# Performance work log

Hardware: AMD Instinct MI355X
Metric: run time of the kernel (lower is better)

The kernel has to match this reference:

```python
import jax, jax.numpy as jnp
import numpy as np

DIM = 1024
HEADS = 16


def setup_inputs() -> dict:
    key = jax.random.key(0)
    ks = jax.random.split(key, 5)
    x = jax.random.normal(ks[0], (2, 2048, DIM), dtype=jnp.float32)
    # nn.Linear init-like scaling
    qkv_w = jax.random.normal(ks[1], (3 * DIM, DIM), dtype=jnp.float32) * (1.0 / np.sqrt(DIM))
    qkv_b = jax.random.normal(ks[2], (3 * DIM,), dtype=jnp.float32) * 0.02
    proj_w = jax.random.normal(ks[3], (DIM, DIM), dtype=jnp.float32) * (1.0 / np.sqrt(DIM))
    proj_b = jax.random.normal(ks[4], (DIM,), dtype=jnp.float32) * 0.02
    return {"x": x, "qkv_w": qkv_w, "qkv_b": qkv_b, "proj_w": proj_w, "proj_b": proj_b}


def reference(x, qkv_w, qkv_b, proj_w, proj_b):
    B, N, C = x.shape
    H = HEADS
    Dh = C // H
    scale = Dh ** -0.5
    # qkv: [B, N, 3C] -> [3, B, H, N, Dh]
    qkv = (x @ qkv_w.T + qkv_b).reshape(B, N, 3, H, Dh).transpose(2, 0, 3, 1, 4)
    q, k, v = qkv[0], qkv[1], qkv[2]
    attn = jnp.einsum('bhnd,bhmd->bhnm', q, k) * scale
    attn = jax.nn.softmax(attn, axis=-1)
    out = jnp.einsum('bhnm,bhmd->bhnd', attn, v)  # [B, H, N, Dh]
    out = out.transpose(0, 2, 1, 3).reshape(B, N, C)
    return out @ proj_w.T + proj_b
```

## Files before the change

### kernel.cpp

```cpp
#include <hip/hip_runtime.h>
#include <stdint.h>

#define DIM    1024
#define NHEADS 16
#define DH     64
#define SEQ    2048
#define BATCH  2
#define BHEADS (BATCH * NHEADS)
#define MROWS  (BATCH * SEQ)
#define SL2E   0.18033688011112042f

typedef __attribute__((ext_vector_type(8))) short bf16x8;
typedef __attribute__((ext_vector_type(4))) float f32x4;
typedef unsigned short ushort_t;

#define GLDS(gp, lp) __builtin_amdgcn_global_load_lds( \
    (__attribute__((address_space(1))) void*)(gp), \
    (__attribute__((address_space(3))) void*)(lp), 16, 0, 0)

__device__ inline ushort_t f2bf(float f) {
    unsigned u = __builtin_bit_cast(unsigned, f);
    u += 0x7FFFu + ((u >> 16) & 1u);
    return (ushort_t)(u >> 16);
}

__global__ __launch_bounds__(256) void cvt_kernel(
    const float* __restrict__ s0, const float* __restrict__ s1, const float* __restrict__ s2,
    ushort_t* __restrict__ d0, ushort_t* __restrict__ d1, ushort_t* __restrict__ d2)
{
    const int N0 = MROWS * DIM;
    const int N1 = 3 * DIM * DIM;
    const int N2 = DIM * DIM;
    int e = (blockIdx.x * 256 + threadIdx.x) << 2;
    const float* src; ushort_t* dst;
    if (e < N0)                { src = s0 + e;             dst = d0 + e; }
    else if (e < N0 + N1)      { src = s1 + (e - N0);      dst = d1 + (e - N0); }
    else if (e < N0 + N1 + N2) { src = s2 + (e - N0 - N1); dst = d2 + (e - N0 - N1); }
    else return;
    float4 f = *(const float4*)src;
    ushort4 o;
    o.x = f2bf(f.x); o.y = f2bf(f.y); o.z = f2bf(f.z); o.w = f2bf(f.w);
    *(ushort4*)dst = o;
}

__global__ __launch_bounds__(256) void qkv_gemm(
    const ushort_t* __restrict__ A, const ushort_t* __restrict__ W,
    const float* __restrict__ bias,
    ushort_t* __restrict__ Qw, ushort_t* __restrict__ Kw, ushort_t* __restrict__ Vt)
{
    __shared__ ushort_t smem[128 * 136];
    ushort_t* As = smem;
    ushort_t* Bs = smem + 128 * 64;

    const int tid  = threadIdx.x;
    const int lane = tid & 63;
    const int wave = tid >> 6;
    const int quad = lane >> 4;
    const int l16  = lane & 15;
    const int wm   = (wave >> 1) * 64;
    const int wn   = (wave & 1) * 64;
    const int bm   = blockIdx.x * 128;
    const int bn   = blockIdx.y * 128;
    const int Rl   = lane >> 3;
    const int pp   = lane & 7;

    f32x4 acc[4][4];
    for (int i = 0; i < 4; i++)
        for (int j = 0; j < 4; j++)
            for (int r = 0; r < 4; r++) acc[i][j][r] = 0.f;

    for (int kk = 0; kk < DIM; kk += 64) {
        __syncthreads();
        for (int j = 0; j < 4; j++) {
            int Rb = j * 32 + wave * 8;
            int R  = Rb + Rl;
            int c  = pp ^ (R & 7);
            GLDS(A + (size_t)(bm + R) * DIM + kk + c * 8, As + Rb * 64 + lane * 8);
            GLDS(W + (size_t)(bn + R) * DIM + kk + c * 8, Bs + Rb * 64 + lane * 8);
        }
        __syncthreads();

        for (int kh = 0; kh < 2; kh++) {
            bf16x8 a[4], b[4];
            for (int mi = 0; mi < 4; mi++) {
                int r = wm + mi * 16 + l16;
                a[mi] = *(const bf16x8*)(As + r * 64 + (((kh * 4 + quad) ^ (r & 7)) << 3));
            }
            for (int ni = 0; ni < 4; ni++) {
                int r = wn + ni * 16 + l16;
                b[ni] = *(const bf16x8*)(Bs + r * 64 + (((kh * 4 + quad) ^ (r & 7)) << 3));
            }
            for (int mi = 0; mi < 4; mi++)
                for (int ni = 0; ni < 4; ni++)
                    acc[mi][ni] = __builtin_amdgcn_mfma_f32_16x16x32_bf16(a[mi], b[ni], acc[mi][ni], 0, 0, 0);
        }
    }

    __syncthreads();
    const int three = bn >> 10;
    const float scale = (three == 0) ? SL2E : 1.0f;
    for (int ni = 0; ni < 4; ni++) {
        int cl   = wn + ni * 16 + l16;
        float bv = bias[bn + cl];
        for (int mi = 0; mi < 4; mi++)
            for (int reg = 0; reg < 4; reg++) {
                int r = wm + mi * 16 + quad * 4 + reg;
                smem[r * 136 + cl] = f2bf((acc[mi][ni][reg] + bv) * scale);
            }
    }
    __syncthreads();

    const int b = bm >> 11, npos0 = bm & 2047;
    if (three < 2) {
        int r = tid >> 1, hh = tid & 1;
        int hc = (bn + hh * 64) & 1023;
        int h  = hc >> 6;
        ushort_t* dst = (three == 0 ? Qw : Kw) + ((size_t)(b * NHEADS + h) * SEQ + npos0 + r) * DH;
        const ushort_t* srcp = smem + r * 136 + hh * 64;
        for (int s = 0; s < 8; s++)
            *(uint4*)(dst + s * 8) = *(const uint4*)(srcp + s * 8);
    } else {
        int c = tid & 127, hh = tid >> 7;
        int hc = (bn + c) & 1023;
        int h  = hc >> 6, d = hc & 63;
        ushort_t* dst = Vt + ((size_t)(b * NHEADS + h) * DH + d) * SEQ + npos0 + hh * 64;
        for (int s = 0; s < 8; s++) {
            union { ushort_t u[8]; uint4 v; } tmp;
            for (int k2 = 0; k2 < 8; k2++)
                tmp.u[k2] = smem[(hh * 64 + s * 8 + k2) * 136 + c];
            *(uint4*)(dst + s * 8) = tmp.v;
        }
    }
}

__global__ __launch_bounds__(512, 4) void attn_kernel(
    const ushort_t* __restrict__ Qw, const ushort_t* __restrict__ Kw,
    const ushort_t* __restrict__ Vt, ushort_t* __restrict__ Ao)
{
    __shared__ ushort_t KV[3][2][64 * 64];
    __shared__ ushort_t QP[8 * 32 * 64];

    const int tid  = threadIdx.x;
    const int lane = tid & 63;
    const int wave = tid >> 6;
    const int quad = lane >> 4;
    const int l16  = lane & 15;
    const int bh   = blockIdx.y;
    const int q0   = blockIdx.x * 256;
    const int Rl   = lane >> 3;
    const int pp   = lane & 7;

    const ushort_t* Qh = Qw + (size_t)bh * SEQ * DH;
    const ushort_t* Kh = Kw + (size_t)bh * SEQ * DH;
    const ushort_t* Vh = Vt + (size_t)bh * DH * SEQ;

    for (int j = 0; j < 4; j++) {
        int Rb = j * 64 + wave * 8;
        int R  = Rb + Rl;
        int c  = pp ^ (R & 7);
        GLDS(Qh + (size_t)(q0 + R) * DH + c * 8, QP + Rb * 64 + lane * 8);
    }
    for (int t = 0; t < 2; t++) {
        int Rb = wave * 8;
        int R  = Rb + Rl;
        int c  = pp ^ (R & 7);
        GLDS(Kh + (size_t)(t * 64 + R) * DH + c * 8,  KV[t][0] + Rb * 64 + lane * 8);
        GLDS(Vh + (size_t)R * SEQ + t * 64 + c * 8,   KV[t][1] + Rb * 64 + lane * 8);
    }
    __syncthreads();

    bf16x8 qf[2][2];
    for (int mi = 0; mi < 2; mi++)
        for (int kh = 0; kh < 2; kh++) {
            int r = wave * 32 + mi * 16 + l16;
            qf[mi][kh] = *(const bf16x8*)(QP + r * 64 + (((kh * 4 + quad) ^ (r & 7)) << 3));
        }
    __syncthreads();

    bf16x8 vones;
    for (int i = 0; i < 8; i++) vones[i] = (short)0x3F80;

    f32x4 oacc[2][4], liacc[2];
    for (int mi = 0; mi < 2; mi++) {
        for (int r = 0; r < 4; r++) liacc[mi][r] = 0.f;
        for (int d = 0; d < 4; d++)
            for (int r = 0; r < 4; r++) oacc[mi][d][r] = 0.f;
    }

    ushort_t* Pw = QP + wave * 32 * 64;

    const int NT = SEQ / 64;
    int cur = 0;
    for (int jt = 0; jt < NT; jt++) {
        if (jt < NT - 2) {
            int pidx = cur + 2; if (pidx >= 3) pidx -= 3;
            int nj0  = (jt + 2) * 64;
            int Rb = wave * 8;
            int R  = Rb + Rl;
            int c  = pp ^ (R & 7);
            GLDS(Kh + (size_t)(nj0 + R) * DH + c * 8,  KV[pidx][0] + Rb * 64 + lane * 8);
            GLDS(Vh + (size_t)R * SEQ + nj0 + c * 8,   KV[pidx][1] + Rb * 64 + lane * 8);
        }
        const ushort_t* Ksb = KV[cur][0];
        const ushort_t* Vsb = KV[cur][1];

        f32x4 s[2][4];
        for (int mi = 0; mi < 2; mi++)
            for (int nf = 0; nf < 4; nf++)
                for (int r = 0; r < 4; r++) s[mi][nf][r] = 0.f;
        for (int kh = 0; kh < 2; kh++)
            for (int nf = 0; nf < 4; nf++) {
                int r = nf * 16 + l16;
                bf16x8 kf = *(const bf16x8*)(Ksb + r * 64 + (((kh * 4 + quad) ^ (r & 7)) << 3));
                s[0][nf] = __builtin_amdgcn_mfma_f32_16x16x32_bf16(kf, qf[0][kh], s[0][nf], 0, 0, 0);
                s[1][nf] = __builtin_amdgcn_mfma_f32_16x16x32_bf16(kf, qf[1][kh], s[1][nf], 0, 0, 0);
            }

        for (int mi = 0; mi < 2; mi++) {
            int row = mi * 16 + l16;
            for (int nf = 0; nf < 4; nf++) {
                unsigned u0 = __builtin_bit_cast(unsigned, __builtin_amdgcn_exp2f(s[mi][nf][0])) + 0x8000u;
                unsigned u1 = __builtin_bit_cast(unsigned, __builtin_amdgcn_exp2f(s[mi][nf][1])) + 0x8000u;
                unsigned u2 = __builtin_bit_cast(unsigned, __builtin_amdgcn_exp2f(s[mi][nf][2])) + 0x8000u;
                unsigned u3 = __builtin_bit_cast(unsigned, __builtin_amdgcn_exp2f(s[mi][nf][3])) + 0x8000u;
                uint2 pk;
                pk.x = __builtin_amdgcn_perm(u1, u0, 0x07060302u);
                pk.y = __builtin_amdgcn_perm(u3, u2, 0x07060302u);
                int j0 = 2 * nf + (quad >> 1);
                int jp = j0 ^ (row & 7);
                *(uint2*)(Pw + row * 64 + jp * 8 + (quad & 1) * 4) = pk;
            }
        }

        bf16x8 pf[2][2];
        for (int mi = 0; mi < 2; mi++) {
            int row = mi * 16 + l16;
            for (int kh = 0; kh < 2; kh++) {
                int jp = (kh * 4 + quad) ^ (row & 7);
                pf[mi][kh] = *(const bf16x8*)(Pw + row * 64 + jp * 8);
            }
        }

        for (int mi = 0; mi < 2; mi++) {
            liacc[mi] = __builtin_amdgcn_mfma_f32_16x16x32_bf16(pf[mi][0], vones, liacc[mi], 0, 0, 0);
            liacc[mi] = __builtin_amdgcn_mfma_f32_16x16x32_bf16(pf[mi][1], vones, liacc[mi], 0, 0, 0);
        }
        for (int kh = 0; kh < 2; kh++)
            for (int df = 0; df < 4; df++) {
                int r = df * 16 + l16;
                bf16x8 vf = *(const bf16x8*)(Vsb + r * 64 + (((kh * 4 + quad) ^ (r & 7)) << 3));
                oacc[0][df] = __builtin_amdgcn_mfma_f32_16x16x32_bf16(pf[0][kh], vf, oacc[0][df], 0, 0, 0);
                oacc[1][df] = __builtin_amdgcn_mfma_f32_16x16x32_bf16(pf[1][kh], vf, oacc[1][df], 0, 0, 0);
            }

        if (jt < NT - 2) {
            __asm volatile("s_waitcnt vmcnt(2)" ::: "memory");
        } else {
            __asm volatile("s_waitcnt vmcnt(0)" ::: "memory");
        }
        __asm volatile("s_barrier" ::: "memory");

        cur++; if (cur == 3) cur = 0;
    }

    const int b = bh >> 4, h = bh & 15;
    for (int mi = 0; mi < 2; mi++)
        for (int r = 0; r < 4; r++) {
            float inv = 1.0f / liacc[mi][r];
            int row = q0 + wave * 32 + mi * 16 + quad * 4 + r;
            for (int df = 0; df < 4; df++) {
                int col = h * 64 + df * 16 + l16;
                Ao[((size_t)b * SEQ + row) * DIM + col] = f2bf(oacc[mi][df][r] * inv);
            }
        }
}

__global__ __launch_bounds__(256, 4) void proj_gemm(
    const ushort_t* __restrict__ A, const ushort_t* __restrict__ W,
    const float* __restrict__ bias, float* __restrict__ Cout)
{
    __shared__ ushort_t As[128 * 64];
    __shared__ ushort_t Bs[64 * 64];

    const int tid  = threadIdx.x;
    const int lane = tid & 63;
    const int wave = tid >> 6;
    const int quad = lane >> 4;
    const int l16  = lane & 15;
    const int wm   = (wave >> 1) * 64;
    const int wn   = (wave & 1) * 32;
    const int bm   = blockIdx.x * 128;
    const int bn   = blockIdx.y * 64;
    const int Rl   = lane >> 3;
    const int pp   = lane & 7;

    f32x4 acc[4][2];
    for (int i = 0; i < 4; i++)
        for (int j = 0; j < 2; j++)
            for (int r = 0; r < 4; r++) acc[i][j][r] = 0.f;

    for (int kk = 0; kk < DIM; kk += 64) {
        __syncthreads();
        for (int j = 0; j < 4; j++) {
            int Rb = j * 32 + wave * 8;
            int R  = Rb + Rl;
            int c  = pp ^ (R & 7);
            GLDS(A + (size_t)(bm + R) * DIM + kk + c * 8, As + Rb * 64 + lane * 8);
        }
        for (int j = 0; j < 2; j++) {
            int Rb = j * 32 + wave * 8;
            int R  = Rb + Rl;
            int c  = pp ^ (R & 7);
            GLDS(W + (size_t)(bn + R) * DIM + kk + c * 8, Bs + Rb * 64 + lane * 8);
        }
        __syncthreads();

        for (int kh = 0; kh < 2; kh++) {
            bf16x8 a[4], b[2];
            for (int mi = 0; mi < 4; mi++) {
                int r = wm + mi * 16 + l16;
                a[mi] = *(const bf16x8*)(As + r * 64 + (((kh * 4 + quad) ^ (r & 7)) << 3));
            }
            for (int ni = 0; ni < 2; ni++) {
                int r = wn + ni * 16 + l16;
                b[ni] = *(const bf16x8*)(Bs + r * 64 + (((kh * 4 + quad) ^ (r & 7)) << 3));
            }
            for (int mi = 0; mi < 4; mi++)
                for (int ni = 0; ni < 2; ni++)
                    acc[mi][ni] = __builtin_amdgcn_mfma_f32_16x16x32_bf16(a[mi], b[ni], acc[mi][ni], 0, 0, 0);
        }
    }

    for (int mi = 0; mi < 4; mi++) {
        for (int ni = 0; ni < 2; ni++) {
            int col  = bn + wn + ni * 16 + l16;
            float bv = bias[col];
            for (int reg = 0; reg < 4; reg++) {
                int row = bm + wm + mi * 16 + quad * 4 + reg;
                Cout[(size_t)row * DIM + col] = acc[mi][ni][reg] + bv;
            }
        }
    }
}

extern "C" void kernel_launch(void* const* d_in, const int* in_sizes, int n_in,
                              void* d_out, int out_size, void* d_ws, size_t ws_size,
                              hipStream_t stream) {
    const float* x      = (const float*)d_in[0];
    const float* qkv_w  = (const float*)d_in[1];
    const float* qkv_b  = (const float*)d_in[2];
    const float* proj_w = (const float*)d_in[3];
    const float* proj_b = (const float*)d_in[4];
    float* out = (float*)d_out;

    ushort_t* xb      = (ushort_t*)d_ws;
    ushort_t* qkv_wb  = xb      + (size_t)MROWS * DIM;
    ushort_t* proj_wb = qkv_wb  + (size_t)3 * DIM * DIM;
    ushort_t* Qw      = proj_wb + (size_t)DIM * DIM;
    ushort_t* Kw      = Qw      + (size_t)BHEADS * SEQ * DH;
    ushort_t* Vt      = Kw      + (size_t)BHEADS * SEQ * DH;
    ushort_t* Ao      = Vt      + (size_t)BHEADS * SEQ * DH;

    const int total_cvt = MROWS * DIM + 3 * DIM * DIM + DIM * DIM;
    cvt_kernel<<<total_cvt / (4 * 256), 256, 0, stream>>>(x, qkv_w, proj_w, xb, qkv_wb, proj_wb);
    qkv_gemm<<<dim3(MROWS / 128, (3 * DIM) / 128), 256, 0, stream>>>(xb, qkv_wb, qkv_b, Qw, Kw, Vt);
    attn_kernel<<<dim3(SEQ / 256, BHEADS), 512, 0, stream>>>(Qw, Kw, Vt, Ao);
    proj_gemm<<<dim3(MROWS / 128, DIM / 64), 256, 0, stream>>>(Ao, proj_wb, proj_b, out);
}
```

Baseline: 203.4 us.

## Split attention KV sequence across two wave groups with LDS reduction

The attention block now covers 128 query rows instead of 256. Its 8 waves form two groups of four, and each group processes alternating 32-key chunks of the sequence. Partial outputs and row sums are then combined through shared memory at the end. This doubles the grid size for better CU occupancy and halves per-block LDS. In exchange it adds a final LDS reduction, uses full block syncs each iteration in place of the triple-buffered vmcnt wait, and loads K/V tiles twice as often per query.

```diff
diff --git a/kernel.cpp b/kernel.cpp
--- a/kernel.cpp
+++ b/kernel.cpp
@@ -133,20 +133,30 @@
     }
 }
 
+struct AttnSmem {
+    ushort_t KV[2][2][2][32 * 64];
+    ushort_t QP[128 * 64];
+};
+union AttnSmemU {
+    AttnSmem m;
+    float Lb[128][66];
+};
+
 __global__ __launch_bounds__(512, 4) void attn_kernel(
     const ushort_t* __restrict__ Qw, const ushort_t* __restrict__ Kw,
     const ushort_t* __restrict__ Vt, ushort_t* __restrict__ Ao)
 {
-    __shared__ ushort_t KV[3][2][64 * 64];
-    __shared__ ushort_t QP[8 * 32 * 64];
+    __shared__ AttnSmemU sh;
 
     const int tid  = threadIdx.x;
     const int lane = tid & 63;
     const int wave = tid >> 6;
+    const int grp  = wave >> 2;
+    const int wg   = wave & 3;
     const int quad = lane >> 4;
     const int l16  = lane & 15;
     const int bh   = blockIdx.y;
-    const int q0   = blockIdx.x * 256;
+    const int q0   = blockIdx.x * 128;
     const int Rl   = lane >> 3;
     const int pp   = lane & 7;
 
@@ -154,26 +164,29 @@
     const ushort_t* Kh = Kw + (size_t)bh * SEQ * DH;
     const ushort_t* Vh = Vt + (size_t)bh * DH * SEQ;
 
-    for (int j = 0; j < 4; j++) {
+    for (int j = 0; j < 2; j++) {
         int Rb = j * 64 + wave * 8;
         int R  = Rb + Rl;
         int c  = pp ^ (R & 7);
-        GLDS(Qh + (size_t)(q0 + R) * DH + c * 8, QP + Rb * 64 + lane * 8);
-    }
-    for (int t = 0; t < 2; t++) {
-        int Rb = wave * 8;
-        int R  = Rb + Rl;
-        int c  = pp ^ (R & 7);
-        GLDS(Kh + (size_t)(t * 64 + R) * DH + c * 8,  KV[t][0] + Rb * 64 + lane * 8);
-        GLDS(Vh + (size_t)R * SEQ + t * 64 + c * 8,   KV[t][1] + Rb * 64 + lane * 8);
+        GLDS(Qh + (size_t)(q0 + R) * DH + c * 8, sh.m.QP + Rb * 64 + lane * 8);
+    }
+    {
+        int t  = grp;
+        int Rk = wg * 8 + Rl;
+        int ck = pp ^ (Rk & 7);
+        GLDS(Kh + (size_t)(t * 32 + Rk) * DH + ck * 8, sh.m.KV[0][grp][0] + wg * 512 + lane * 8);
+        int Rv = wg * 16 + (lane >> 2);
+        int pv = lane & 3;
+        int cv = pv ^ ((Rv >> 1) & 3);
+        GLDS(Vh + (size_t)Rv * SEQ + t * 32 + cv * 8, sh.m.KV[0][grp][1] + wg * 512 + lane * 8);
     }
     __syncthreads();
 
     bf16x8 qf[2][2];
     for (int mi = 0; mi < 2; mi++)
         for (int kh = 0; kh < 2; kh++) {
-            int r = wave * 32 + mi * 16 + l16;
-            qf[mi][kh] = *(const bf16x8*)(QP + r * 64 + (((kh * 4 + quad) ^ (r & 7)) << 3));
+            int r = wg * 32 + mi * 16 + l16;
+            qf[mi][kh] = *(const bf16x8*)(sh.m.QP + r * 64 + (((kh * 4 + quad) ^ (r & 7)) << 3));
         }
     __syncthreads();
 
@@ -187,29 +200,31 @@
             for (int r = 0; r < 4; r++) oacc[mi][d][r] = 0.f;
     }
 
-    ushort_t* Pw = QP + wave * 32 * 64;
-
-    const int NT = SEQ / 64;
-    int cur = 0;
-    for (int jt = 0; jt < NT; jt++) {
-        if (jt < NT - 2) {
-            int pidx = cur + 2; if (pidx >= 3) pidx -= 3;
-            int nj0  = (jt + 2) * 64;
-            int Rb = wave * 8;
-            int R  = Rb + Rl;
-            int c  = pp ^ (R & 7);
-            GLDS(Kh + (size_t)(nj0 + R) * DH + c * 8,  KV[pidx][0] + Rb * 64 + lane * 8);
-            GLDS(Vh + (size_t)R * SEQ + nj0 + c * 8,   KV[pidx][1] + Rb * 64 + lane * 8);
-        }
-        const ushort_t* Ksb = KV[cur][0];
-        const ushort_t* Vsb = KV[cur][1];
-
-        f32x4 s[2][4];
+    ushort_t* Pw = sh.m.QP + wave * 1024;
+
+    const int NIT = 32;
+    for (int it = 0; it < NIT; it++) {
+        const int phase = it & 1;
+        if (it < NIT - 1) {
+            int np = phase ^ 1;
+            int t  = 2 * (it + 1) + grp;
+            int Rk = wg * 8 + Rl;
+            int ck = pp ^ (Rk & 7);
+            GLDS(Kh + (size_t)(t * 32 + Rk) * DH + ck * 8, sh.m.KV[np][grp][0] + wg * 512 + lane * 8);
+            int Rv = wg * 16 + (lane >> 2);
+            int pv = lane & 3;
+            int cv = pv ^ ((Rv >> 1) & 3);
+            GLDS(Vh + (size_t)Rv * SEQ + t * 32 + cv * 8, sh.m.KV[np][grp][1] + wg * 512 + lane * 8);
+        }
+        const ushort_t* Ksb = sh.m.KV[phase][grp][0];
+        const ushort_t* Vsb = sh.m.KV[phase][grp][1];
+
+        f32x4 s[2][2];
         for (int mi = 0; mi < 2; mi++)
-            for (int nf = 0; nf < 4; nf++)
+            for (int nf = 0; nf < 2; nf++)
                 for (int r = 0; r < 4; r++) s[mi][nf][r] = 0.f;
         for (int kh = 0; kh < 2; kh++)
-            for (int nf = 0; nf < 4; nf++) {
+            for (int nf = 0; nf < 2; nf++) {
                 int r = nf * 16 + l16;
                 bf16x8 kf = *(const bf16x8*)(Ksb + r * 64 + (((kh * 4 + quad) ^ (r & 7)) << 3));
                 s[0][nf] = __builtin_amdgcn_mfma_f32_16x16x32_bf16(kf, qf[0][kh], s[0][nf], 0, 0, 0);
@@ -218,7 +233,8 @@
 
         for (int mi = 0; mi < 2; mi++) {
             int row = mi * 16 + l16;
-            for (int nf = 0; nf < 4; nf++) {
+            int swz = (row >> 1) & 3;
+            for (int nf = 0; nf < 2; nf++) {
                 unsigned u0 = __builtin_bit_cast(unsigned, __builtin_amdgcn_exp2f(s[mi][nf][0])) + 0x8000u;
                 unsigned u1 = __builtin_bit_cast(unsigned, __builtin_amdgcn_exp2f(s[mi][nf][1])) + 0x8000u;
                 unsigned u2 = __builtin_bit_cast(unsigned, __builtin_amdgcn_exp2f(s[mi][nf][2])) + 0x8000u;
@@ -226,53 +242,56 @@
                 uint2 pk;
                 pk.x = __builtin_amdgcn_perm(u1, u0, 0x07060302u);
                 pk.y = __builtin_amdgcn_perm(u3, u2, 0x07060302u);
-                int j0 = 2 * nf + (quad >> 1);
-                int jp = j0 ^ (row & 7);
-                *(uint2*)(Pw + row * 64 + jp * 8 + (quad & 1) * 4) = pk;
-            }
-        }
-
-        bf16x8 pf[2][2];
+                int jp = (nf * 2 + (quad >> 1)) ^ swz;
+                *(uint2*)(Pw + row * 32 + jp * 8 + (quad & 1) * 4) = pk;
+            }
+        }
+
+        bf16x8 pf[2];
         for (int mi = 0; mi < 2; mi++) {
             int row = mi * 16 + l16;
-            for (int kh = 0; kh < 2; kh++) {
-                int jp = (kh * 4 + quad) ^ (row & 7);
-                pf[mi][kh] = *(const bf16x8*)(Pw + row * 64 + jp * 8);
-            }
-        }
-
-        for (int mi = 0; mi < 2; mi++) {
-            liacc[mi] = __builtin_amdgcn_mfma_f32_16x16x32_bf16(pf[mi][0], vones, liacc[mi], 0, 0, 0);
-            liacc[mi] = __builtin_amdgcn_mfma_f32_16x16x32_bf16(pf[mi][1], vones, liacc[mi], 0, 0, 0);
-        }
-        for (int kh = 0; kh < 2; kh++)
-            for (int df = 0; df < 4; df++) {
-                int r = df * 16 + l16;
-                bf16x8 vf = *(const bf16x8*)(Vsb + r * 64 + (((kh * 4 + quad) ^ (r & 7)) << 3));
-                oacc[0][df] = __builtin_amdgcn_mfma_f32_16x16x32_bf16(pf[0][kh], vf, oacc[0][df], 0, 0, 0);
-                oacc[1][df] = __builtin_amdgcn_mfma_f32_16x16x32_bf16(pf[1][kh], vf, oacc[1][df], 0, 0, 0);
-            }
-
-        if (jt < NT - 2) {
-            __asm volatile("s_waitcnt vmcnt(2)" ::: "memory");
-        } else {
-            __asm volatile("s_waitcnt vmcnt(0)" ::: "memory");
-        }
-        __asm volatile("s_barrier" ::: "memory");
-
-        cur++; if (cur == 3) cur = 0;
+            int jp  = quad ^ ((row >> 1) & 3);
+            pf[mi] = *(const bf16x8*)(Pw + row * 32 + jp * 8);
+        }
+
+        liacc[0] = __builtin_amdgcn_mfma_f32_16x16x32_bf16(pf[0], vones, liacc[0], 0, 0, 0);
+        liacc[1] = __builtin_amdgcn_mfma_f32_16x16x32_bf16(pf[1], vones, liacc[1], 0, 0, 0);
+
+        for (int df = 0; df < 4; df++) {
+            int r  = df * 16 + l16;
+            int jp = quad ^ ((r >> 1) & 3);
+            bf16x8 vf = *(const bf16x8*)(Vsb + r * 32 + jp * 8);
+            oacc[0][df] = __builtin_amdgcn_mfma_f32_16x16x32_bf16(pf[0], vf, oacc[0][df], 0, 0, 0);
+            oacc[1][df] = __builtin_amdgcn_mfma_f32_16x16x32_bf16(pf[1], vf, oacc[1][df], 0, 0, 0);
+        }
+
+        __syncthreads();
     }
 
     const int b = bh >> 4, h = bh & 15;
-    for (int mi = 0; mi < 2; mi++)
-        for (int r = 0; r < 4; r++) {
-            float inv = 1.0f / liacc[mi][r];
-            int row = q0 + wave * 32 + mi * 16 + quad * 4 + r;
-            for (int df = 0; df < 4; df++) {
-                int col = h * 64 + df * 16 + l16;
-                Ao[((size_t)b * SEQ + row) * DIM + col] = f2bf(oacc[mi][df][r] * inv);
-            }
-        }
+    if (grp == 1) {
+        for (int mi = 0; mi < 2; mi++)
+            for (int reg = 0; reg < 4; reg++) {
+                int row = wg * 32 + mi * 16 + quad * 4 + reg;
+                for (int df = 0; df < 4; df++)
+                    sh.Lb[row][df * 16 + l16] = oacc[mi][df][reg];
+                if (l16 == 0) sh.Lb[row][64] = liacc[mi][reg];
+            }
+    }
+    __syncthreads();
+    if (grp == 0) {
+        for (int mi = 0; mi < 2; mi++)
+            for (int reg = 0; reg < 4; reg++) {
+                int row   = wg * 32 + mi * 16 + quad * 4 + reg;
+                float inv = 1.0f / (liacc[mi][reg] + sh.Lb[row][64]);
+                int grow  = q0 + row;
+                for (int df = 0; df < 4; df++) {
+                    int col = df * 16 + l16;
+                    float o = oacc[mi][df][reg] + sh.Lb[row][col];
+                    Ao[((size_t)b * SEQ + grow) * DIM + h * 64 + col] = f2bf(o * inv);
+                }
+            }
+    }
 }
 
 __global__ __launch_bounds__(256, 4) void proj_gemm(
@@ -364,6 +383,6 @@
     const int total_cvt = MROWS * DIM + 3 * DIM * DIM + DIM * DIM;
     cvt_kernel<<<total_cvt / (4 * 256), 256, 0, stream>>>(x, qkv_w, proj_w, xb, qkv_wb, proj_wb);
     qkv_gemm<<<dim3(MROWS / 128, (3 * DIM) / 128), 256, 0, stream>>>(xb, qkv_wb, qkv_b, Qw, Kw, Vt);
-    attn_kernel<<<dim3(SEQ / 256, BHEADS), 512, 0, stream>>>(Qw, Kw, Vt, Ao);
+    attn_kernel<<<dim3(SEQ / 128, BHEADS), 512, 0, stream>>>(Qw, Kw, Vt, Ao);
     proj_gemm<<<dim3(MROWS / 128, DIM / 64), 256, 0, stream>>>(Ao, proj_wb, proj_b, out);
 }
```

Result: faster. 190.5 us (-6.4%).
